# Optimization experiments

Hardware: AMD Instinct MI355X
Metric: run time of the kernel (lower is better)

The kernel has to match this reference:

```python
import jax, jax.numpy as jnp
import numpy as np
from jax import lax

CHUNK = 32

def _l2norm(x, eps=1e-6):
    # matches fla l2norm: x / ||x||_2 along last dim
    return x * lax.rsqrt(jnp.sum(x * x, axis=-1, keepdims=True) + eps)

def _delta_rule_chunkwise(q, k, v, beta, chunk=CHUNK):
    b, h, L, dk = q.shape
    dv = v.shape[-1]
    pad = (-L) % chunk
    if pad:
        pw = ((0, 0), (0, 0), (0, pad), (0, 0))
        q = jnp.pad(q, pw); k = jnp.pad(k, pw); v = jnp.pad(v, pw)
        beta = jnp.pad(beta, ((0, 0), (0, 0), (0, pad)))
    Lp = L + pad
    n = Lp // chunk

    q = _l2norm(q)
    k = _l2norm(k)
    v = v * beta[..., None]
    k_beta = k * beta[..., None]

    # [b,h,n,c,d]
    rs = lambda t: t.reshape(b, h, n, chunk, t.shape[-1])
    qc, kc, vc, kbc = rs(q), rs(k), rs(v), rs(k_beta)

    idx = jnp.arange(chunk)
    strict_lower = (idx[:, None] > idx[None, :])           # used for inv
    lower_incl = (idx[:, None] >= idx[None, :])            # used for attn_local

    # inv = -(k_beta k^T), keep strictly-lower part only
    inv = jnp.where(strict_lower, -jnp.einsum('bhnid,bhnjd->bhnij', kbc, kc), 0.0)
    # sequential forward substitution: inv[i,:i] += inv[i,:] @ inv[:,:i]
    for i in range(1, chunk):
        row = inv[..., i, :]                                # [b,h,n,c]
        upd = jnp.einsum('bhnk,bhnkc->bhnc', row, inv)      # contributions from rows < i
        inv = inv.at[..., i, :].add(jnp.where(idx < i, upd, 0.0))
    inv = inv + jnp.eye(chunk, dtype=inv.dtype)

    u = jnp.einsum('bhnij,bhnjd->bhnid', inv, vc)           # [b,h,n,c,dv]
    w = jnp.einsum('bhnij,bhnjd->bhnid', inv, kbc)          # [b,h,n,c,dk]

    S0 = jnp.zeros((b, h, dk, dv), dtype=q.dtype)

    def step(S, blk):
        q_i, k_i, u_i0, w_i = blk
        attn = jnp.where(lower_incl, jnp.einsum('bhid,bhjd->bhij', q_i, k_i), 0.0)
        u_i = u_i0 - jnp.einsum('bhik,bhkd->bhid', w_i, S)
        o = jnp.einsum('bhik,bhkd->bhid', q_i, S) + jnp.einsum('bhij,bhjd->bhid', attn, u_i)
        S = S + jnp.einsum('bhci,bhcd->bhid', k_i, u_i)
        return S, o

    mv = lambda t: jnp.moveaxis(t, 2, 0)                    # [n,b,h,c,d]
    S, outs = lax.scan(step, S0, (mv(qc), mv(kc), mv(u), mv(w)))
    out = jnp.moveaxis(outs, 0, 2).reshape(b, h, Lp, dv)
    if pad:
        out = out[:, :, :L]
    return out, S

def setup_inputs() -> dict:
    key = jax.random.key(0)
    kq, kk, kv, kb = jax.random.split(key, 4)
    b, h, L, d = 2, 16, 4096, 128
    q = jax.random.normal(kq, (b, h, L, d), dtype=jnp.float32)
    k = jax.random.normal(kk, (b, h, L, d), dtype=jnp.float32)
    v = jax.random.normal(kv, (b, h, L, d), dtype=jnp.float32)
    beta = jax.random.uniform(kb, (b, h, L), dtype=jnp.float32)
    return {"q": q, "k": k, "v": v, "beta": beta}

def reference(q, k, v, beta):
    return _delta_rule_chunkwise(q, k, v, beta)
```

## Files before the change

### kernel.cpp

```cpp
#include <hip/hip_runtime.h>
#include <math.h>

#define BH   32
#define LSEQ 4096
#define DK   128
#define DV   128
#define CH   32
#define NC   (LSEQ/CH)

typedef float4 f4;
typedef unsigned short u16;
typedef __attribute__((ext_vector_type(8))) short  bf16x8;
typedef __attribute__((ext_vector_type(4))) float  f32x4;

#define MFMA16(a,b,c) __builtin_amdgcn_mfma_f32_16x16x32_bf16((a),(b),(c),0,0,0)

__device__ __forceinline__ float dot4(const f4 a, const f4 b) {
    return a.x*b.x + a.y*b.y + a.z*b.z + a.w*b.w;
}
__device__ __forceinline__ unsigned pk2(float a, float b) {
    unsigned ua = __builtin_bit_cast(unsigned, a);
    unsigned ub = __builtin_bit_cast(unsigned, b);
    ua = (ua + 0x7FFFu + ((ua >> 16) & 1u)) >> 16;
    ub = (ub + 0x7FFFu + ((ub >> 16) & 1u)) >> 16;
    return (ua & 0xFFFFu) | (ub << 16);
}
__device__ __forceinline__ u16 bf1(float a) {
    unsigned ua = __builtin_bit_cast(unsigned, a);
    ua = (ua + 0x7FFFu + ((ua >> 16) & 1u)) >> 16;
    return (u16)ua;
}
__device__ __forceinline__ unsigned cvtpk(float a, float b) {
    unsigned r;
    asm("v_cvt_pk_bf16_f32 %0, %1, %2" : "=v"(r) : "v"(a), "v"(b));
    return r;
}

__global__ __launch_bounds__(256) void prep_kernel(
    const float* __restrict__ q, const float* __restrict__ k, float* __restrict__ v,
    const float* __restrict__ beta,
    u16* __restrict__ qb16, u16* __restrict__ wb16,
    u16* __restrict__ kT16, u16* __restrict__ A16)
{
    __shared__ u16 qn[CH][136];
    __shared__ u16 kn[CH][136];
    __shared__ u16 vT[DK][40];
    __shared__ u16 knT[DK][40];
    __shared__ float Ts[CH][33];
    __shared__ float Af[CH][33];
    __shared__ u16 Tb[CH][40];
    __shared__ float redq[CH][8], redk[CH][8];
    __shared__ float bet[CH], scq[CH], sck[CH];

    const int tid = threadIdx.x;
    const int hh  = blockIdx.x >> 7;
    const int c   = blockIdx.x & (NC-1);
    const size_t rowbase = (size_t)hh * LSEQ + (size_t)c * CH;
    const size_t base    = rowbase * DK;
    const size_t tb      = (size_t)(hh * NC + c);

    const int r = tid >> 3, sub = tid & 7, d0 = sub * 16;
    const int wid = tid >> 6, lane = tid & 63, quad = lane >> 4, m16 = lane & 15;

    f4 tq[4], tk[4], tv[4];
    float sq = 0.f, sk = 0.f;
#pragma unroll
    for (int m = 0; m < 4; ++m) {
        tq[m] = *(const f4*)(q + base + (size_t)r*DK + d0 + m*4);
        tk[m] = *(const f4*)(k + base + (size_t)r*DK + d0 + m*4);
        tv[m] = *(const f4*)(v + base + (size_t)r*DK + d0 + m*4);
        sq += dot4(tq[m], tq[m]);
        sk += dot4(tk[m], tk[m]);
    }
    redq[r][sub] = sq;
    redk[r][sub] = sk;
    if (tid < CH) bet[tid] = beta[rowbase + tid];
    __syncthreads();
    if (tid < CH) {
        float a = 0.f, b = 0.f;
#pragma unroll
        for (int j = 0; j < 8; ++j) { a += redq[tid][j]; b += redk[tid][j]; }
        scq[tid] = 1.0f / sqrtf(a + 1e-6f);
        sck[tid] = 1.0f / sqrtf(b + 1e-6f);
    }
    __syncthreads();
    const float aq = scq[r], ak = sck[r];
#pragma unroll
    for (int m = 0; m < 4; ++m) {
        tq[m].x *= aq; tq[m].y *= aq; tq[m].z *= aq; tq[m].w *= aq;
        tk[m].x *= ak; tk[m].y *= ak; tk[m].z *= ak; tk[m].w *= ak;
    }
    {
        uint4 p0, p1;
        p0.x = pk2(tq[0].x,tq[0].y); p0.y = pk2(tq[0].z,tq[0].w);
        p0.z = pk2(tq[1].x,tq[1].y); p0.w = pk2(tq[1].z,tq[1].w);
        p1.x = pk2(tq[2].x,tq[2].y); p1.y = pk2(tq[2].z,tq[2].w);
        p1.z = pk2(tq[3].x,tq[3].y); p1.w = pk2(tq[3].z,tq[3].w);
        *(uint4*)&qn[r][d0]     = p0;  *(uint4*)&qn[r][d0+8] = p1;
        const int qf = ((r>>4)*4 + (sub>>1))*512 + ((r&15) + (sub&1)*32)*8;
        *(uint4*)(qb16 + tb*4096 + qf)       = p0;
        *(uint4*)(qb16 + tb*4096 + qf + 128) = p1;
        uint4 k0, k1;
        k0.x = pk2(tk[0].x,tk[0].y); k0.y = pk2(tk[0].z,tk[0].w);
        k0.z = pk2(tk[1].x,tk[1].y); k0.w = pk2(tk[1].z,tk[1].w);
        k1.x = pk2(tk[2].x,tk[2].y); k1.y = pk2(tk[2].z,tk[2].w);
        k1.z = pk2(tk[3].x,tk[3].y); k1.w = pk2(tk[3].z,tk[3].w);
        *(uint4*)&kn[r][d0]     = k0;  *(uint4*)&kn[r][d0+8] = k1;
    }
#pragma unroll
    for (int m = 0; m < 4; ++m) {
        knT[d0+m*4+0][r] = bf1(tk[m].x); knT[d0+m*4+1][r] = bf1(tk[m].y);
        knT[d0+m*4+2][r] = bf1(tk[m].z); knT[d0+m*4+3][r] = bf1(tk[m].w);
        vT [d0+m*4+0][r] = bf1(tv[m].x); vT [d0+m*4+1][r] = bf1(tv[m].y);
        vT [d0+m*4+2][r] = bf1(tv[m].z); vT [d0+m*4+3][r] = bf1(tv[m].w);
    }
    __syncthreads();

    {
        const int d = tid >> 1, jh = (tid & 1) * 16;
        uint4 z0 = *(const uint4*)&knT[d][jh];
        uint4 z1 = *(const uint4*)&knT[d][jh+8];
        const int kf = (d>>4)*512 + ((d&15) + (tid&1)*32)*8;
        *(uint4*)(kT16 + tb*4096 + kf)       = z0;
        *(uint4*)(kT16 + tb*4096 + kf + 128) = z1;
    }
    {
        const int ti = wid >> 1, tj = wid & 1;
        f32x4 aA = {0.f,0.f,0.f,0.f}, aG = {0.f,0.f,0.f,0.f};
#pragma unroll
        for (int ks = 0; ks < 4; ++ks) {
            bf16x8 xq = *(const bf16x8*)&qn[ti*16+m16][ks*32 + quad*8];
            bf16x8 xk = *(const bf16x8*)&kn[ti*16+m16][ks*32 + quad*8];
            bf16x8 yk = *(const bf16x8*)&kn[tj*16+m16][ks*32 + quad*8];
            aA = MFMA16(xq, yk, aA);
            aG = MFMA16(xk, yk, aG);
        }
#pragma unroll
        for (int reg = 0; reg < 4; ++reg) {
            Af[ti*16 + quad*4 + reg][tj*16 + m16] = aA[reg];
            Ts[ti*16 + quad*4 + reg][tj*16 + m16] = aG[reg];
        }
    }
    __syncthreads();

    {
        const int i = r, j0 = sub * 4;
        float a[4];
#pragma unroll
        for (int jj = 0; jj < 4; ++jj)
            a[jj] = (j0+jj <= i) ? Af[i][j0+jj] : 0.f;
        uint2 pa; pa.x = pk2(a[0], a[1]); pa.y = pk2(a[2], a[3]);
        const int af = (i>>4)*512 + ((i&15) + (sub>>1)*16)*8 + (sub&1)*4;
        *(uint2*)(A16 + tb*1024 + af) = pa;
        const float bi = bet[i];
#pragma unroll
        for (int jj = 0; jj < 4; ++jj) {
            const int j = j0 + jj;
            const float gv = Ts[i][j];
            Ts[i][j] = (j < i) ? -bi * gv : 0.f;
        }
    }
    __syncthreads();

    if (tid < 32) {
        float rr[32];
#pragma unroll
        for (int i = 0; i < 32; ++i) rr[i] = Ts[i][tid];
#pragma unroll
        for (int i = 1; i < 32; ++i) {
            float t = 0.f;
#pragma unroll
            for (int kk = 0; kk < i; ++kk)
                t += __shfl(rr[i], kk) * rr[kk];
            rr[i] += t;
        }
        const float bj = bet[tid];
#pragma unroll
        for (int i = 0; i < 32; ++i)
            Ts[i][tid] = ((i == tid) ? 1.0f : rr[i]) * bj;
    }
    __syncthreads();
    {
        const int i = r, j0 = sub * 4;
        uint2 p; p.x = pk2(Ts[i][j0], Ts[i][j0+1]); p.y = pk2(Ts[i][j0+2], Ts[i][j0+3]);
        *(uint2*)&Tb[i][j0] = p;
    }
    __syncthreads();

#pragma unroll
    for (int dt = 0; dt < 2; ++dt)
#pragma unroll
    for (int it = 0; it < 2; ++it) {
        const int drow = wid*32 + dt*16 + m16;
        bf16x8 av  = *(const bf16x8*)&vT[drow][quad*8];
        bf16x8 ak2 = *(const bf16x8*)&knT[drow][quad*8];
        bf16x8 bT  = *(const bf16x8*)&Tb[it*16 + m16][quad*8];
        f32x4 aU = {0.f,0.f,0.f,0.f}, aW = {0.f,0.f,0.f,0.f};
        aU = MFMA16(av,  bT, aU);
        aW = MFMA16(ak2, bT, aW);
        const int ii = it*16 + m16;
        const int dd = wid*32 + dt*16 + quad*4;
        f4 us; us.x = aU[0]; us.y = aU[1]; us.z = aU[2]; us.w = aU[3];
        *(f4*)(v + base + (size_t)ii*DK + dd) = us;
        uint2 pw; pw.x = pk2(-aW[0], -aW[1]); pw.y = pk2(-aW[2], -aW[3]);
        const int wf = (it*4 + wid)*512 + (m16 + (dt*2 + (quad>>1))*16)*8 + (quad&1)*4;
        *(uint2*)(wb16 + tb*4096 + wf) = pw;
    }
}

__global__ __launch_bounds__(64) void scan_kernel(
    const u16* __restrict__ qb16, const u16* __restrict__ wb16,
    const u16* __restrict__ kT16, const u16* __restrict__ A16,
    const float* __restrict__ u0, float* __restrict__ out)
{
    __shared__ u16 STl[16*128];

    const int lane = threadIdx.x;
    const int quad = lane >> 4, m16 = lane & 15;
    const int hh = blockIdx.x & 31, g = blockIdx.x >> 5;

    const u16* wg = wb16 + (size_t)hh * NC * 4096 + lane*8;
    const u16* qg = qb16 + (size_t)hh * NC * 4096 + lane*8;
    const u16* kg = kT16 + (size_t)hh * NC * 4096 + lane*8;
    const u16* Ag = A16  + (size_t)hh * NC * 1024 + lane*8;
    const float* ug = u0 + (size_t)hh * LSEQ * DK + (size_t)(quad*4)*DK + g*16 + m16;
    float* og = out + (size_t)hh * LSEQ * DV + (size_t)(quad*4)*DV + g*16 + m16;

    const int swz = (m16 & 7) << 3;

    bf16x8 WA[8], KA[8], QA[8], AA[2];
    f32x4 U0r[2];
    f32x4 SA[8];
    bf16x8 SB[4];
#pragma unroll
    for (int t = 0; t < 8; ++t) SA[t] = (f32x4){0.f,0.f,0.f,0.f};
#pragma unroll
    for (int ks = 0; ks < 4; ++ks) SB[ks] = (bf16x8){};

#define LOADWU(cc) do { \
    const u16* wp_ = wg + (size_t)(cc)*4096; \
    _Pragma("unroll") \
    for (int f = 0; f < 8; ++f) WA[f] = *(const bf16x8*)(wp_ + f*512); \
    const float* up_ = ug + (size_t)(cc)*CH*DK; \
    _Pragma("unroll") \
    for (int r2 = 0; r2 < 4; ++r2) { \
        U0r[0][r2] = up_[(size_t)r2*DK]; \
        U0r[1][r2] = up_[(size_t)(16+r2)*DK]; } \
} while (0)
#define LOADK(cc) do { \
    const u16* kp_ = kg + (size_t)(cc)*4096; \
    _Pragma("unroll") \
    for (int f = 0; f < 8; ++f) KA[f] = *(const bf16x8*)(kp_ + f*512); \
} while (0)
#define LOADQ(cc) do { \
    const u16* qp_ = qg + (size_t)(cc)*4096; \
    _Pragma("unroll") \
    for (int f = 0; f < 8; ++f) QA[f] = *(const bf16x8*)(qp_ + f*512); \
    const u16* ap_ = Ag + (size_t)(cc)*1024; \
    AA[0] = *(const bf16x8*)(ap_); \
    AA[1] = *(const bf16x8*)(ap_ + 512); \
} while (0)

    LOADWU(0); LOADK(0); LOADQ(0);

    for (int c = 0; c < NC; ++c) {
        const int cn = (c + 1 < NC) ? c + 1 : c;

        f32x4 ua0 = U0r[0], ua1 = U0r[1];
        f32x4 ub0 = {0.f,0.f,0.f,0.f}, ub1 = {0.f,0.f,0.f,0.f};
        ua0 = MFMA16(WA[0], SB[0], ua0);  ub0 = MFMA16(WA[1], SB[1], ub0);
        ua0 = MFMA16(WA[2], SB[2], ua0);  ub0 = MFMA16(WA[3], SB[3], ub0);
        ua1 = MFMA16(WA[4], SB[0], ua1);  ub1 = MFMA16(WA[5], SB[1], ub1);
        ua1 = MFMA16(WA[6], SB[2], ua1);  ub1 = MFMA16(WA[7], SB[3], ub1);
        ua0 += ub0;  ua1 += ub1;

        LOADWU(cn);

        const unsigned Wa0 = cvtpk(ua0[0], ua0[1]), Wa1 = cvtpk(ua0[2], ua0[3]);
        const unsigned Wb0 = cvtpk(ua1[0], ua1[1]), Wb1 = cvtpk(ua1[2], ua1[3]);
        const int s0l = ((quad & 1) << 5) + m16, s1l = s0l + 16;
        union { unsigned w[4]; bf16x8 v; } uc;
        {
            const unsigned a0 = __shfl((int)Wa0, s0l), b0 = __shfl((int)Wb0, s0l);
            const unsigned a1 = __shfl((int)Wa1, s0l), b1 = __shfl((int)Wb1, s0l);
            const unsigned a2 = __shfl((int)Wa0, s1l), b2 = __shfl((int)Wb0, s1l);
            const unsigned a3 = __shfl((int)Wa1, s1l), b3 = __shfl((int)Wb1, s1l);
            const bool hi = (quad >= 2);
            uc.w[0] = hi ? b0 : a0; uc.w[1] = hi ? b1 : a1;
            uc.w[2] = hi ? b2 : a2; uc.w[3] = hi ? b3 : a3;
        }
        const bf16x8 UB = uc.v;

#pragma unroll
        for (int t = 0; t < 8; ++t)
            SA[t] = MFMA16(KA[t], UB, SA[t]);

        LOADK(cn);

        f32x4 za0 = {0.f,0.f,0.f,0.f}, zb0 = {0.f,0.f,0.f,0.f};
        f32x4 za1 = {0.f,0.f,0.f,0.f}, zb1 = {0.f,0.f,0.f,0.f};
        za0 = MFMA16(QA[0], SB[0], za0);  zb0 = MFMA16(QA[1], SB[1], zb0);
        za0 = MFMA16(QA[2], SB[2], za0);  zb0 = MFMA16(QA[3], SB[3], zb0);
        za1 = MFMA16(QA[4], SB[0], za1);  zb1 = MFMA16(QA[5], SB[1], zb1);
        za1 = MFMA16(QA[6], SB[2], za1);  zb1 = MFMA16(QA[7], SB[3], zb1);
        za0 += zb0;  za1 += zb1;
        za0 = MFMA16(AA[0], UB, za0);
        za1 = MFMA16(AA[1], UB, za1);
        {
            float* o0 = og + (size_t)c * CH * DV;
            o0[0] = za0[0]; o0[DV] = za0[1]; o0[2*DV] = za0[2]; o0[3*DV] = za0[3];
            float* o1 = o0 + (size_t)16 * DV;
            o1[0] = za1[0]; o1[DV] = za1[1]; o1[2*DV] = za1[2]; o1[3*DV] = za1[3];
        }

        LOADQ(cn);

#pragma unroll
        for (int t = 0; t < 8; ++t) {
            uint2 p;
            p.x = cvtpk(SA[t][0], SA[t][1]);
            p.y = cvtpk(SA[t][2], SA[t][3]);
            *(uint2*)&STl[(m16*128 + t*16 + quad*4) ^ swz] = p;
        }
#pragma unroll
        for (int ks = 0; ks < 4; ++ks)
            SB[ks] = *(const bf16x8*)&STl[(m16*128 + ks*32 + quad*8) ^ swz];
    }

    {
        float* sg = out + (size_t)BH*LSEQ*DV
                        + ((size_t)hh*DK + quad*4)*DV + g*16 + m16;
#pragma unroll
        for (int t = 0; t < 8; ++t) {
            float* sp = sg + (size_t)t * 16 * DV;
            sp[0] = SA[t][0]; sp[DV] = SA[t][1]; sp[2*DV] = SA[t][2]; sp[3*DV] = SA[t][3];
        }
    }
#undef LOADQ
#undef LOADK
#undef LOADWU
}

extern "C" void kernel_launch(void* const* d_in, const int* in_sizes, int n_in,
                              void* d_out, int out_size, void* d_ws, size_t ws_size,
                              hipStream_t stream) {
    (void)in_sizes; (void)n_in; (void)out_size; (void)ws_size;
    const float* q = (const float*)d_in[0];
    const float* k = (const float*)d_in[1];
    float* v = (float*)d_in[2];
    const float* beta = (const float*)d_in[3];
    float* out = (float*)d_out;

    const size_t NE = (size_t)BH * LSEQ * DK;
    u16* qb16 = (u16*)d_ws;
    u16* wb16 = qb16 + NE;
    u16* kT16 = wb16 + NE;
    u16* A16  = kT16 + NE;

    prep_kernel<<<dim3(BH*NC), dim3(256), 0, stream>>>(q, k, v, beta, qb16, wb16, kT16, A16);
    scan_kernel<<<dim3(256), dim3(64), 0, stream>>>(qb16, wb16, kT16, A16, v, out);
}
```

Measured before the change: 411.5 us.

## Prefetch scan operands via async global-to-LDS loads with triple buffering

```diff
diff --git a/kernel.cpp b/kernel.cpp
--- a/kernel.cpp
+++ b/kernel.cpp
@@ -15,6 +15,9 @@
 
 #define MFMA16(a,b,c) __builtin_amdgcn_mfma_f32_16x16x32_bf16((a),(b),(c),0,0,0)
 
+#define AS1 __attribute__((address_space(1)))
+#define AS3 __attribute__((address_space(3)))
+
 __device__ __forceinline__ float dot4(const f4 a, const f4 b) {
     return a.x*b.x + a.y*b.y + a.z*b.z + a.w*b.w;
 }
@@ -34,6 +37,12 @@
     unsigned r;
     asm("v_cvt_pk_bf16_f32 %0, %1, %2" : "=v"(r) : "v"(a), "v"(b));
     return r;
+}
+__device__ __forceinline__ void gl16(const u16* g, u16* l) {
+    __builtin_amdgcn_global_load_lds((const AS1 void*)g, (AS3 void*)l, 16, 0, 0);
+}
+__device__ __forceinline__ void gl4(const float* g, u16* l) {
+    __builtin_amdgcn_global_load_lds((const AS1 void*)g, (AS3 void*)l, 4, 0, 0);
 }
 
 __global__ __launch_bounds__(256) void prep_kernel(
@@ -213,6 +222,7 @@
     const u16* __restrict__ kT16, const u16* __restrict__ A16,
     const float* __restrict__ u0, float* __restrict__ out)
 {
+    __shared__ u16 stg[3][14336];
     __shared__ u16 STl[16*128];
 
     const int lane = threadIdx.x;
@@ -228,44 +238,49 @@
 
     const int swz = (m16 & 7) << 3;
 
-    bf16x8 WA[8], KA[8], QA[8], AA[2];
-    f32x4 U0r[2];
     f32x4 SA[8];
     bf16x8 SB[4];
+    bf16x8 WA[8], KA[8];
+    f32x4 U0r[2];
 #pragma unroll
     for (int t = 0; t < 8; ++t) SA[t] = (f32x4){0.f,0.f,0.f,0.f};
 #pragma unroll
     for (int ks = 0; ks < 4; ++ks) SB[ks] = (bf16x8){};
 
-#define LOADWU(cc) do { \
+#define ISSUE(bb, cc) do { \
+    asm volatile("" ::: "memory");  \
+    u16* s_ = &stg[bb][0]; \
     const u16* wp_ = wg + (size_t)(cc)*4096; \
-    _Pragma("unroll") \
-    for (int f = 0; f < 8; ++f) WA[f] = *(const bf16x8*)(wp_ + f*512); \
+    const u16* kp_ = kg + (size_t)(cc)*4096; \
+    const u16* qp_ = qg + (size_t)(cc)*4096; \
+    const u16* ap_ = Ag + (size_t)(cc)*1024; \
     const float* up_ = ug + (size_t)(cc)*CH*DK; \
-    _Pragma("unroll") \
-    for (int r2 = 0; r2 < 4; ++r2) { \
-        U0r[0][r2] = up_[(size_t)r2*DK]; \
-        U0r[1][r2] = up_[(size_t)(16+r2)*DK]; } \
+    _Pragma("unroll") for (int f_ = 0; f_ < 8; ++f_) gl16(wp_ + f_*512, s_ + f_*512); \
+    _Pragma("unroll") for (int f_ = 0; f_ < 8; ++f_) gl16(kp_ + f_*512, s_ + 4096 + f_*512); \
+    _Pragma("unroll") for (int f_ = 0; f_ < 8; ++f_) gl16(qp_ + f_*512, s_ + 8192 + f_*512); \
+    gl16(ap_,       s_ + 12288); \
+    gl16(ap_ + 512, s_ + 12800); \
+    _Pragma("unroll") for (int p_ = 0; p_ < 8; ++p_) \
+        gl4(up_ + (size_t)((p_>>2)*16 + (p_&3))*DK, s_ + 13312 + p_*128); \
 } while (0)
-#define LOADK(cc) do { \
-    const u16* kp_ = kg + (size_t)(cc)*4096; \
-    _Pragma("unroll") \
-    for (int f = 0; f < 8; ++f) KA[f] = *(const bf16x8*)(kp_ + f*512); \
+
+#define RDNEXT(bb) do { \
+    const u16* s_ = &stg[bb][0]; \
+    _Pragma("unroll") for (int f_ = 0; f_ < 8; ++f_) \
+        WA[f_] = *(const bf16x8*)(s_ + f_*512 + lane*8); \
+    _Pragma("unroll") for (int f_ = 0; f_ < 8; ++f_) \
+        KA[f_] = *(const bf16x8*)(s_ + 4096 + f_*512 + lane*8); \
+    _Pragma("unroll") for (int p_ = 0; p_ < 8; ++p_) \
+        U0r[p_>>2][p_&3] = *(const float*)(s_ + 13312 + p_*128 + lane*2); \
 } while (0)
-#define LOADQ(cc) do { \
-    const u16* qp_ = qg + (size_t)(cc)*4096; \
-    _Pragma("unroll") \
-    for (int f = 0; f < 8; ++f) QA[f] = *(const bf16x8*)(qp_ + f*512); \
-    const u16* ap_ = Ag + (size_t)(cc)*1024; \
-    AA[0] = *(const bf16x8*)(ap_); \
-    AA[1] = *(const bf16x8*)(ap_ + 512); \
-} while (0)
-
-    LOADWU(0); LOADK(0); LOADQ(0);
-
+
+    ISSUE(0, 0);
+    ISSUE(1, 1);
+    asm volatile("s_waitcnt vmcnt(34)" ::: "memory");
+    RDNEXT(0);
+
+    int b = 0, b1 = 1, b2 = 2;
     for (int c = 0; c < NC; ++c) {
-        const int cn = (c + 1 < NC) ? c + 1 : c;
-
         f32x4 ua0 = U0r[0], ua1 = U0r[1];
         f32x4 ub0 = {0.f,0.f,0.f,0.f}, ub1 = {0.f,0.f,0.f,0.f};
         ua0 = MFMA16(WA[0], SB[0], ua0);  ub0 = MFMA16(WA[1], SB[1], ub0);
@@ -274,20 +289,20 @@
         ua1 = MFMA16(WA[6], SB[2], ua1);  ub1 = MFMA16(WA[7], SB[3], ub1);
         ua0 += ub0;  ua1 += ub1;
 
-        LOADWU(cn);
+        { const int cn2 = (c + 2 < NC) ? c + 2 : NC - 1; ISSUE(b2, cn2); }
 
         const unsigned Wa0 = cvtpk(ua0[0], ua0[1]), Wa1 = cvtpk(ua0[2], ua0[3]);
         const unsigned Wb0 = cvtpk(ua1[0], ua1[1]), Wb1 = cvtpk(ua1[2], ua1[3]);
         const int s0l = ((quad & 1) << 5) + m16, s1l = s0l + 16;
         union { unsigned w[4]; bf16x8 v; } uc;
         {
-            const unsigned a0 = __shfl((int)Wa0, s0l), b0 = __shfl((int)Wb0, s0l);
-            const unsigned a1 = __shfl((int)Wa1, s0l), b1 = __shfl((int)Wb1, s0l);
-            const unsigned a2 = __shfl((int)Wa0, s1l), b2 = __shfl((int)Wb0, s1l);
-            const unsigned a3 = __shfl((int)Wa1, s1l), b3 = __shfl((int)Wb1, s1l);
+            const unsigned a0 = __shfl((int)Wa0, s0l), b0_ = __shfl((int)Wb0, s0l);
+            const unsigned a1 = __shfl((int)Wa1, s0l), b1_ = __shfl((int)Wb1, s0l);
+            const unsigned a2 = __shfl((int)Wa0, s1l), b2_ = __shfl((int)Wb0, s1l);
+            const unsigned a3 = __shfl((int)Wa1, s1l), b3_ = __shfl((int)Wb1, s1l);
             const bool hi = (quad >= 2);
-            uc.w[0] = hi ? b0 : a0; uc.w[1] = hi ? b1 : a1;
-            uc.w[2] = hi ? b2 : a2; uc.w[3] = hi ? b3 : a3;
+            uc.w[0] = hi ? b0_ : a0; uc.w[1] = hi ? b1_ : a1;
+            uc.w[2] = hi ? b2_ : a2; uc.w[3] = hi ? b3_ : a3;
         }
         const bf16x8 UB = uc.v;
 
@@ -295,7 +310,29 @@
         for (int t = 0; t < 8; ++t)
             SA[t] = MFMA16(KA[t], UB, SA[t]);
 
-        LOADK(cn);
+#pragma unroll
+        for (int t = 0; t < 8; ++t) {
+            uint2 p;
+            p.x = cvtpk(SA[t][0], SA[t][1]);
+            p.y = cvtpk(SA[t][2], SA[t][3]);
+            *(uint2*)&STl[(m16*128 + t*16 + quad*4) ^ swz] = p;
+        }
+
+        asm volatile("s_waitcnt vmcnt(34)" ::: "memory");
+
+        bf16x8 QA[8], AA0, AA1, SBn[4];
+        {
+            const u16* s_ = &stg[b][0];
+#pragma unroll
+            for (int f_ = 0; f_ < 8; ++f_)
+                QA[f_] = *(const bf16x8*)(s_ + 8192 + f_*512 + lane*8);
+            AA0 = *(const bf16x8*)(s_ + 12288 + lane*8);
+            AA1 = *(const bf16x8*)(s_ + 12800 + lane*8);
+        }
+#pragma unroll
+        for (int ks = 0; ks < 4; ++ks)
+            SBn[ks] = *(const bf16x8*)&STl[(m16*128 + ks*32 + quad*8) ^ swz];
+        RDNEXT(b1);
 
         f32x4 za0 = {0.f,0.f,0.f,0.f}, zb0 = {0.f,0.f,0.f,0.f};
         f32x4 za1 = {0.f,0.f,0.f,0.f}, zb1 = {0.f,0.f,0.f,0.f};
@@ -304,8 +341,8 @@
         za1 = MFMA16(QA[4], SB[0], za1);  zb1 = MFMA16(QA[5], SB[1], zb1);
         za1 = MFMA16(QA[6], SB[2], za1);  zb1 = MFMA16(QA[7], SB[3], zb1);
         za0 += zb0;  za1 += zb1;
-        za0 = MFMA16(AA[0], UB, za0);
-        za1 = MFMA16(AA[1], UB, za1);
+        za0 = MFMA16(AA0, UB, za0);
+        za1 = MFMA16(AA1, UB, za1);
         {
             float* o0 = og + (size_t)c * CH * DV;
             o0[0] = za0[0]; o0[DV] = za0[1]; o0[2*DV] = za0[2]; o0[3*DV] = za0[3];
@@ -313,18 +350,9 @@
             o1[0] = za1[0]; o1[DV] = za1[1]; o1[2*DV] = za1[2]; o1[3*DV] = za1[3];
         }
 
-        LOADQ(cn);
-
-#pragma unroll
-        for (int t = 0; t < 8; ++t) {
-            uint2 p;
-            p.x = cvtpk(SA[t][0], SA[t][1]);
-            p.y = cvtpk(SA[t][2], SA[t][3]);
-            *(uint2*)&STl[(m16*128 + t*16 + quad*4) ^ swz] = p;
-        }
-#pragma unroll
-        for (int ks = 0; ks < 4; ++ks)
-            SB[ks] = *(const bf16x8*)&STl[(m16*128 + ks*32 + quad*8) ^ swz];
+#pragma unroll
+        for (int ks = 0; ks < 4; ++ks) SB[ks] = SBn[ks];
+        { const int bt = b; b = b1; b1 = b2; b2 = bt; }
     }
 
     {
@@ -336,9 +364,8 @@
             sp[0] = SA[t][0]; sp[DV] = SA[t][1]; sp[2*DV] = SA[t][2]; sp[3*DV] = SA[t][3];
         }
     }
-#undef LOADQ
-#undef LOADK
-#undef LOADWU
+#undef RDNEXT
+#undef ISSUE
 }
 
 extern "C" void kernel_launch(void* const* d_in, const int* in_sizes, int n_in,
```

After: 436.7 us. +6.1%, slower.

## Warp-specialize scan kernel: producer waves stage W/K/U, separate wave computes outputs

Applied to the files above, without the earlier changes.

```diff
diff --git a/kernel.cpp b/kernel.cpp
--- a/kernel.cpp
+++ b/kernel.cpp
@@ -208,126 +208,180 @@
     }
 }
 
-__global__ __launch_bounds__(64) void scan_kernel(
+__global__ __launch_bounds__(256, 1) void scan_kernel(
     const u16* __restrict__ qb16, const u16* __restrict__ wb16,
     const u16* __restrict__ kT16, const u16* __restrict__ A16,
     const float* __restrict__ u0, float* __restrict__ out)
 {
-    __shared__ u16 STl[16*128];
-
-    const int lane = threadIdx.x;
+    __shared__ u16   stgW[3][4096];
+    __shared__ u16   stgK[3][4096];
+    __shared__ float stgU[3][576];
+    __shared__ u16   STs[2][4608];
+
+    const int tid  = threadIdx.x;
+    const int wid  = tid >> 6;
+    const int lane = tid & 63;
     const int quad = lane >> 4, m16 = lane & 15;
-    const int hh = blockIdx.x & 31, g = blockIdx.x >> 5;
+    const int hh   = blockIdx.x & 31, g = blockIdx.x >> 5;
 
     const u16* wg = wb16 + (size_t)hh * NC * 4096 + lane*8;
+    const u16* kg = kT16 + (size_t)hh * NC * 4096 + lane*8;
     const u16* qg = qb16 + (size_t)hh * NC * 4096 + lane*8;
-    const u16* kg = kT16 + (size_t)hh * NC * 4096 + lane*8;
     const u16* Ag = A16  + (size_t)hh * NC * 1024 + lane*8;
-    const float* ug = u0 + (size_t)hh * LSEQ * DK + (size_t)(quad*4)*DK + g*16 + m16;
+    const float* ugl = u0 + (size_t)hh * LSEQ * DK + g*16 + m16;
     float* og = out + (size_t)hh * LSEQ * DV + (size_t)(quad*4)*DV + g*16 + m16;
 
     const int swz = (m16 & 7) << 3;
 
-    bf16x8 WA[8], KA[8], QA[8], AA[2];
-    f32x4 U0r[2];
-    f32x4 SA[8];
-    bf16x8 SB[4];
+    f32x4 SA[8]; bf16x8 SB[4];
+    bf16x8 WAO[8], WAE[8], KAO[8], KAE[8];
+    f32x4 U0O[2], U0E[2];
+    bf16x8 QAO[8], QAE[8], AAO[2], AAE[2];
+    uint4 sldO[8], sldE[8];
+    float uldO[8], uldE[8];
+
 #pragma unroll
     for (int t = 0; t < 8; ++t) SA[t] = (f32x4){0.f,0.f,0.f,0.f};
 #pragma unroll
-    for (int ks = 0; ks < 4; ++ks) SB[ks] = (bf16x8){};
-
-#define LOADWU(cc) do { \
-    const u16* wp_ = wg + (size_t)(cc)*4096; \
-    _Pragma("unroll") \
-    for (int f = 0; f < 8; ++f) WA[f] = *(const bf16x8*)(wp_ + f*512); \
-    const float* up_ = ug + (size_t)(cc)*CH*DK; \
-    _Pragma("unroll") \
-    for (int r2 = 0; r2 < 4; ++r2) { \
-        U0r[0][r2] = up_[(size_t)r2*DK]; \
-        U0r[1][r2] = up_[(size_t)(16+r2)*DK]; } \
-} while (0)
-#define LOADK(cc) do { \
-    const u16* kp_ = kg + (size_t)(cc)*4096; \
-    _Pragma("unroll") \
-    for (int f = 0; f < 8; ++f) KA[f] = *(const bf16x8*)(kp_ + f*512); \
-} while (0)
-#define LOADQ(cc) do { \
+    for (int k = 0; k < 4; ++k) SB[k] = (bf16x8){};
+
+#define RAWBAR() do { \
+    asm volatile("s_waitcnt lgkmcnt(0)" ::: "memory"); \
+    __builtin_amdgcn_s_barrier(); \
+    __builtin_amdgcn_sched_barrier(0); \
+} while (0)
+
+#define SPREF(P, cc) do { \
+    if (wid == 2) { \
+        const u16* p_ = wg + (size_t)(cc)*4096; \
+        _Pragma("unroll") for (int f_ = 0; f_ < 8; ++f_) \
+            sld##P[f_] = *(const uint4*)(p_ + f_*512); \
+        _Pragma("unroll") for (int j_ = 0; j_ < 8; ++j_) \
+            uld##P[j_] = ugl[(size_t)((cc)*CH + quad*8 + j_)*DK]; \
+    } else if (wid == 3) { \
+        const u16* p_ = kg + (size_t)(cc)*4096; \
+        _Pragma("unroll") for (int f_ = 0; f_ < 8; ++f_) \
+            sld##P[f_] = *(const uint4*)(p_ + f_*512); \
+    } \
+} while (0)
+
+#define SSTAGE(P, bw_) do { \
+    if (wid == 2) { \
+        _Pragma("unroll") for (int f_ = 0; f_ < 8; ++f_) \
+            *(uint4*)&stgW[bw_][f_*512 + lane*8] = sld##P[f_]; \
+        float4 t0_, t1_; \
+        t0_.x = uld##P[0]; t0_.y = uld##P[1]; t0_.z = uld##P[2]; t0_.w = uld##P[3]; \
+        t1_.x = uld##P[4]; t1_.y = uld##P[5]; t1_.z = uld##P[6]; t1_.w = uld##P[7]; \
+        *(float4*)&stgU[bw_][m16*36 + quad*8]     = t0_; \
+        *(float4*)&stgU[bw_][m16*36 + quad*8 + 4] = t1_; \
+    } else if (wid == 3) { \
+        _Pragma("unroll") for (int f_ = 0; f_ < 8; ++f_) \
+            *(uint4*)&stgK[bw_][f_*512 + lane*8] = sld##P[f_]; \
+    } \
+} while (0)
+
+#define W0READ(P, br_) do { \
+    _Pragma("unroll") for (int f_ = 0; f_ < 8; ++f_) \
+        WA##P[f_] = *(const bf16x8*)&stgW[br_][f_*512 + lane*8]; \
+    _Pragma("unroll") for (int f_ = 0; f_ < 8; ++f_) \
+        KA##P[f_] = *(const bf16x8*)&stgK[br_][f_*512 + lane*8]; \
+    U0##P[0] = *(const f32x4*)&stgU[br_][m16*36 + quad*4]; \
+    U0##P[1] = *(const f32x4*)&stgU[br_][m16*36 + 16 + quad*4]; \
+} while (0)
+
+#define QPREF(P, cc) do { \
     const u16* qp_ = qg + (size_t)(cc)*4096; \
-    _Pragma("unroll") \
-    for (int f = 0; f < 8; ++f) QA[f] = *(const bf16x8*)(qp_ + f*512); \
-    const u16* ap_ = Ag + (size_t)(cc)*1024; \
-    AA[0] = *(const bf16x8*)(ap_); \
-    AA[1] = *(const bf16x8*)(ap_ + 512); \
-} while (0)
-
-    LOADWU(0); LOADK(0); LOADQ(0);
-
-    for (int c = 0; c < NC; ++c) {
-        const int cn = (c + 1 < NC) ? c + 1 : c;
-
-        f32x4 ua0 = U0r[0], ua1 = U0r[1];
-        f32x4 ub0 = {0.f,0.f,0.f,0.f}, ub1 = {0.f,0.f,0.f,0.f};
-        ua0 = MFMA16(WA[0], SB[0], ua0);  ub0 = MFMA16(WA[1], SB[1], ub0);
-        ua0 = MFMA16(WA[2], SB[2], ua0);  ub0 = MFMA16(WA[3], SB[3], ub0);
-        ua1 = MFMA16(WA[4], SB[0], ua1);  ub1 = MFMA16(WA[5], SB[1], ub1);
-        ua1 = MFMA16(WA[6], SB[2], ua1);  ub1 = MFMA16(WA[7], SB[3], ub1);
-        ua0 += ub0;  ua1 += ub1;
-
-        LOADWU(cn);
-
-        const unsigned Wa0 = cvtpk(ua0[0], ua0[1]), Wa1 = cvtpk(ua0[2], ua0[3]);
-        const unsigned Wb0 = cvtpk(ua1[0], ua1[1]), Wb1 = cvtpk(ua1[2], ua1[3]);
-        const int s0l = ((quad & 1) << 5) + m16, s1l = s0l + 16;
-        union { unsigned w[4]; bf16x8 v; } uc;
-        {
-            const unsigned a0 = __shfl((int)Wa0, s0l), b0 = __shfl((int)Wb0, s0l);
-            const unsigned a1 = __shfl((int)Wa1, s0l), b1 = __shfl((int)Wb1, s0l);
-            const unsigned a2 = __shfl((int)Wa0, s1l), b2 = __shfl((int)Wb0, s1l);
-            const unsigned a3 = __shfl((int)Wa1, s1l), b3 = __shfl((int)Wb1, s1l);
-            const bool hi = (quad >= 2);
-            uc.w[0] = hi ? b0 : a0; uc.w[1] = hi ? b1 : a1;
-            uc.w[2] = hi ? b2 : a2; uc.w[3] = hi ? b3 : a3;
-        }
-        const bf16x8 UB = uc.v;
-
-#pragma unroll
-        for (int t = 0; t < 8; ++t)
-            SA[t] = MFMA16(KA[t], UB, SA[t]);
-
-        LOADK(cn);
-
-        f32x4 za0 = {0.f,0.f,0.f,0.f}, zb0 = {0.f,0.f,0.f,0.f};
-        f32x4 za1 = {0.f,0.f,0.f,0.f}, zb1 = {0.f,0.f,0.f,0.f};
-        za0 = MFMA16(QA[0], SB[0], za0);  zb0 = MFMA16(QA[1], SB[1], zb0);
-        za0 = MFMA16(QA[2], SB[2], za0);  zb0 = MFMA16(QA[3], SB[3], zb0);
-        za1 = MFMA16(QA[4], SB[0], za1);  zb1 = MFMA16(QA[5], SB[1], zb1);
-        za1 = MFMA16(QA[6], SB[2], za1);  zb1 = MFMA16(QA[7], SB[3], zb1);
-        za0 += zb0;  za1 += zb1;
-        za0 = MFMA16(AA[0], UB, za0);
-        za1 = MFMA16(AA[1], UB, za1);
-        {
-            float* o0 = og + (size_t)c * CH * DV;
-            o0[0] = za0[0]; o0[DV] = za0[1]; o0[2*DV] = za0[2]; o0[3*DV] = za0[3];
-            float* o1 = o0 + (size_t)16 * DV;
-            o1[0] = za1[0]; o1[DV] = za1[1]; o1[2*DV] = za1[2]; o1[3*DV] = za1[3];
-        }
-
-        LOADQ(cn);
-
-#pragma unroll
-        for (int t = 0; t < 8; ++t) {
-            uint2 p;
-            p.x = cvtpk(SA[t][0], SA[t][1]);
-            p.y = cvtpk(SA[t][2], SA[t][3]);
-            *(uint2*)&STl[(m16*128 + t*16 + quad*4) ^ swz] = p;
-        }
-#pragma unroll
-        for (int ks = 0; ks < 4; ++ks)
-            SB[ks] = *(const bf16x8*)&STl[(m16*128 + ks*32 + quad*8) ^ swz];
-    }
-
-    {
+    _Pragma("unroll") for (int f_ = 0; f_ < 8; ++f_) \
+        QA##P[f_] = *(const bf16x8*)(qp_ + f_*512); \
+    AA##P[0] = *(const bf16x8*)(Ag + (size_t)(cc)*1024); \
+    AA##P[1] = *(const bf16x8*)(Ag + (size_t)(cc)*1024 + 512); \
+} while (0)
+
+    SPREF(O, 0);  SSTAGE(O, 0);
+    SPREF(O, 1);  SSTAGE(O, 1);
+    SPREF(O, 2);
+    SPREF(E, 3);
+    if (wid == 1) { QPREF(O, 0); QPREF(E, 1); }
+    RAWBAR();
+    if (wid == 0) { W0READ(O, 0); }
+
+#define BODY(c_, CUR, NXT) do { \
+    if (wid == 0) { \
+        if ((c_) < NC) { \
+            u16* st_ = &STs[(c_) & 1][0]; \
+            _Pragma("unroll") for (int f_ = 0; f_ < 4; ++f_) \
+                *(bf16x8*)(st_ + f_*512 + lane*8) = SB[f_];             \
+            if ((c_) + 1 < NC) { W0READ(NXT, ((c_)+1) % 3); }            \
+             \
+            f32x4 ua0 = U0##CUR[0], ua1 = U0##CUR[1]; \
+            f32x4 ub0 = {0.f,0.f,0.f,0.f}, ub1 = {0.f,0.f,0.f,0.f}; \
+            ua0 = MFMA16(WA##CUR[0], SB[0], ua0);  ub0 = MFMA16(WA##CUR[1], SB[1], ub0); \
+            ua0 = MFMA16(WA##CUR[2], SB[2], ua0);  ub0 = MFMA16(WA##CUR[3], SB[3], ub0); \
+            ua1 = MFMA16(WA##CUR[4], SB[0], ua1);  ub1 = MFMA16(WA##CUR[5], SB[1], ub1); \
+            ua1 = MFMA16(WA##CUR[6], SB[2], ua1);  ub1 = MFMA16(WA##CUR[7], SB[3], ub1); \
+            ua0[0]+=ub0[0]; ua0[1]+=ub0[1]; ua0[2]+=ub0[2]; ua0[3]+=ub0[3]; \
+            ua1[0]+=ub1[0]; ua1[1]+=ub1[1]; ua1[2]+=ub1[2]; ua1[3]+=ub1[3]; \
+             \
+            const unsigned Wa0 = cvtpk(ua0[0], ua0[1]), Wa1 = cvtpk(ua0[2], ua0[3]); \
+            const unsigned Wb0 = cvtpk(ua1[0], ua1[1]), Wb1 = cvtpk(ua1[2], ua1[3]); \
+            const int s0l_ = ((quad & 1) << 5) + m16, s1l_ = s0l_ + 16; \
+            union { unsigned w[4]; bf16x8 v; } uc_; \
+            { const unsigned a0_ = __shfl((int)Wa0, s0l_), b0_ = __shfl((int)Wb0, s0l_); \
+              const unsigned a1_ = __shfl((int)Wa1, s0l_), b1_ = __shfl((int)Wb1, s0l_); \
+              const unsigned a2_ = __shfl((int)Wa0, s1l_), b2_ = __shfl((int)Wb0, s1l_); \
+              const unsigned a3_ = __shfl((int)Wa1, s1l_), b3_ = __shfl((int)Wb1, s1l_); \
+              const bool hi_ = (quad >= 2); \
+              uc_.w[0] = hi_ ? b0_ : a0_; uc_.w[1] = hi_ ? b1_ : a1_; \
+              uc_.w[2] = hi_ ? b2_ : a2_; uc_.w[3] = hi_ ? b3_ : a3_; } \
+            const bf16x8 UB_ = uc_.v; \
+            *(bf16x8*)(st_ + 2048 + lane*8) = UB_;                       \
+             \
+            _Pragma("unroll") for (int t_ = 0; t_ < 8; ++t_) \
+                SA[t_] = MFMA16(KA##CUR[t_], UB_, SA[t_]); \
+             \
+            _Pragma("unroll") for (int t_ = 0; t_ < 8; ++t_) { \
+                uint2 p_; p_.x = cvtpk(SA[t_][0], SA[t_][1]); p_.y = cvtpk(SA[t_][2], SA[t_][3]); \
+                *(uint2*)&st_[2560 + ((m16*128 + t_*16 + quad*4) ^ swz)] = p_; } \
+            _Pragma("unroll") for (int k_ = 0; k_ < 4; ++k_) \
+                SB[k_] = *(const bf16x8*)&st_[2560 + ((m16*128 + k_*32 + quad*8) ^ swz)]; \
+        } \
+    } else if (wid == 1) { \
+        if ((c_) >= 1 && (c_) <= NC) { \
+            const u16* st_ = &STs[((c_) - 1) & 1][0]; \
+            bf16x8 sb0_ = *(const bf16x8*)(st_ + 0*512 + lane*8); \
+            bf16x8 sb1_ = *(const bf16x8*)(st_ + 1*512 + lane*8); \
+            bf16x8 sb2_ = *(const bf16x8*)(st_ + 2*512 + lane*8); \
+            bf16x8 sb3_ = *(const bf16x8*)(st_ + 3*512 + lane*8); \
+            bf16x8 ub_  = *(const bf16x8*)(st_ + 2048 + lane*8); \
+            f32x4 za0 = {0.f,0.f,0.f,0.f}, zb0 = {0.f,0.f,0.f,0.f}; \
+            f32x4 za1 = {0.f,0.f,0.f,0.f}, zb1 = {0.f,0.f,0.f,0.f}; \
+            za0 = MFMA16(QA##NXT[0], sb0_, za0);  zb0 = MFMA16(QA##NXT[1], sb1_, zb0); \
+            za0 = MFMA16(QA##NXT[2], sb2_, za0);  zb0 = MFMA16(QA##NXT[3], sb3_, zb0); \
+            za1 = MFMA16(QA##NXT[4], sb0_, za1);  zb1 = MFMA16(QA##NXT[5], sb1_, zb1); \
+            za1 = MFMA16(QA##NXT[6], sb2_, za1);  zb1 = MFMA16(QA##NXT[7], sb3_, zb1); \
+            za0[0]+=zb0[0]; za0[1]+=zb0[1]; za0[2]+=zb0[2]; za0[3]+=zb0[3]; \
+            za1[0]+=zb1[0]; za1[1]+=zb1[1]; za1[2]+=zb1[2]; za1[3]+=zb1[3]; \
+            za0 = MFMA16(AA##NXT[0], ub_, za0); \
+            za1 = MFMA16(AA##NXT[1], ub_, za1); \
+            float* o0_ = og + (size_t)((c_) - 1) * CH * DV; \
+            o0_[0] = za0[0]; o0_[DV] = za0[1]; o0_[2*DV] = za0[2]; o0_[3*DV] = za0[3]; \
+            float* o1_ = o0_ + (size_t)16 * DV; \
+            o1_[0] = za1[0]; o1_[DV] = za1[1]; o1_[2*DV] = za1[2]; o1_[3*DV] = za1[3]; \
+        } \
+        if ((c_) + 1 < NC) { QPREF(NXT, (c_) + 1); } \
+    } else { \
+        if ((c_) + 2 < NC) SSTAGE(CUR, ((c_) + 2) % 3); \
+        if ((c_) + 4 < NC) SPREF(CUR, (c_) + 4); \
+    } \
+    RAWBAR(); \
+} while (0)
+
+    for (int c = 0; c < NC + 2; c += 2) {
+        BODY(c,     O, E);
+        BODY(c + 1, E, O);
+    }
+
+    if (wid == 0) {
         float* sg = out + (size_t)BH*LSEQ*DV
                         + ((size_t)hh*DK + quad*4)*DV + g*16 + m16;
 #pragma unroll
@@ -336,9 +390,12 @@
             sp[0] = SA[t][0]; sp[DV] = SA[t][1]; sp[2*DV] = SA[t][2]; sp[3*DV] = SA[t][3];
         }
     }
-#undef LOADQ
-#undef LOADK
-#undef LOADWU
+#undef BODY
+#undef QPREF
+#undef W0READ
+#undef SSTAGE
+#undef SPREF
+#undef RAWBAR
 }
 
 extern "C" void kernel_launch(void* const* d_in, const int* in_sizes, int n_in,
@@ -358,5 +415,5 @@
     u16* A16  = kT16 + NE;
 
     prep_kernel<<<dim3(BH*NC), dim3(256), 0, stream>>>(q, k, v, beta, qb16, wb16, kT16, A16);
-    scan_kernel<<<dim3(256), dim3(64), 0, stream>>>(qb16, wb16, kT16, A16, v, out);
-}
+    scan_kernel<<<dim3(256), dim3(256), 0, stream>>>(qb16, wb16, kT16, A16, v, out);
+}
```

New measurement: 870.1 us. 111% more time.
